# Kernel tuning notes

Hardware: AMD Instinct MI355X
Metric: run time of the kernel (lower is better)

The kernel has to match this reference:

```python
import jax, jax.numpy as jnp
import numpy as np


def setup_inputs() -> dict:
    key = jax.random.key(0)
    ks = jax.random.split(key, 8)
    B, L, E, U = 32, 2048, 1024, 1024
    s = 0.02
    return {
        "dec_hidden": jax.random.normal(ks[0], (B, E), jnp.float32),
        "enc_output": jax.random.normal(ks[1], (B, L, E), jnp.float32),
        "prev_coverage": jax.random.uniform(ks[2], (B, L, 1), jnp.float32),
        "Ws_k": jax.random.normal(ks[3], (E, U), jnp.float32) * s,
        "Ws_b": jnp.zeros((U,), jnp.float32),
        "Wh_k": jax.random.normal(ks[4], (E, U), jnp.float32) * s,
        "Wh_b": jnp.zeros((U,), jnp.float32),
        "Wc_k": jax.random.normal(ks[5], (1, U), jnp.float32) * s,
        "Wc_b": jnp.zeros((U,), jnp.float32),
        "V_k": jax.random.normal(ks[6], (U, 1), jnp.float32) * s,
        "V_b": jnp.zeros((1,), jnp.float32),
        "enc_pad_mask": jnp.ones((B, L), jnp.int32),
        "use_coverage": 1,
    }


def reference(dec_hidden, enc_output, prev_coverage, Ws_k, Ws_b, Wh_k, Wh_b,
              Wc_k, Wc_b, V_k, V_b, enc_pad_mask, use_coverage):
    # projections: [B,L,U] + [B,1,U] (+ [B,L,U] coverage term)
    pre = jnp.einsum('ble,eu->blu', enc_output, Ws_k) + Ws_b \
        + (dec_hidden @ Wh_k + Wh_b)[:, None, :]
    if use_coverage:
        pre = pre + (prev_coverage @ Wc_k + Wc_b)
    score = jnp.tanh(pre) @ V_k + V_b              # [B, L, 1]
    mask = enc_pad_mask.astype(score.dtype)        # [B, L]
    masked_score = (score[..., 0] * mask)[..., None]  # [B, L, 1]
    attention_weights = jax.nn.softmax(masked_score, axis=1)
    coverage = attention_weights + prev_coverage if use_coverage else attention_weights
    context_vector = jnp.sum(attention_weights * enc_output, axis=1)  # [B, E]
    return (context_vector, attention_weights, coverage)
```

## Files before the change

### kernel.cpp

```cpp
#include <hip/hip_runtime.h>
#include <hip/hip_bf16.h>
#include <math.h>

typedef float f32x4 __attribute__((ext_vector_type(4)));
typedef short short8 __attribute__((ext_vector_type(8)));
typedef unsigned short u16x8 __attribute__((ext_vector_type(8)));

static __device__ __forceinline__ unsigned short f2bf(float f) {
    unsigned u = __builtin_bit_cast(unsigned, f);
    unsigned r = (u + 0x7FFFu + ((u >> 16) & 1u)) >> 16;
    return (unsigned short)r;
}
static __device__ __forceinline__ float bf2f(unsigned short h) {
    unsigned u = ((unsigned)h) << 16;
    return __builtin_bit_cast(float, u);
}
static __device__ __forceinline__ float fast_tanh(float x) {
    float ax = fminf(fmaxf(x, -9.f), 9.f);
    float e = __expf(2.f * ax);
    return 1.f - 2.f / (e + 1.f);
}

#define GLD16(g, l) __builtin_amdgcn_global_load_lds(                        \
    (const __attribute__((address_space(1))) void*)(g),                      \
    (__attribute__((address_space(3))) void*)(l), 16, 0, 0)

__global__ __launch_bounds__(256) void prep_kernel(
    const float* __restrict__ enc, unsigned short* __restrict__ encB,
    const float* __restrict__ ws, unsigned short* __restrict__ wst,
    const float* __restrict__ dh, const float* __restrict__ whk,
    float* __restrict__ base_part)
{
    __shared__ unsigned short tile[64][65];
    __shared__ float dS[128];
    const int bid = blockIdx.x, tid = threadIdx.x;

    if (bid < 16384) {
        const size_t base0 = (size_t)bid * 4096;
#pragma unroll
        for (int i = 0; i < 4; i++) {
            size_t g = base0 + (size_t)i * 1024 + tid * 4;
            f32x4 v = *(const f32x4*)(enc + g);
            ushort4 w;
            w.x = f2bf(v.x); w.y = f2bf(v.y); w.z = f2bf(v.z); w.w = f2bf(v.w);
            *(ushort4*)(encB + g) = w;
        }
    } else if (bid < 16640) {
        const int b2 = bid - 16384;
        const int e0 = (b2 & 15) * 64, u0 = (b2 >> 4) * 64;
#pragma unroll
        for (int i = 0; i < 16; i++) {
            int idx = i * 256 + tid;
            int r = idx >> 6, c = idx & 63;
            tile[r][c] = f2bf(ws[(size_t)(e0 + r) * 1024 + u0 + c]);
        }
        __syncthreads();
#pragma unroll
        for (int i = 0; i < 16; i++) {
            int idx = i * 256 + tid;
            int r = idx >> 6, c = idx & 63;
            wst[(size_t)(u0 + r) * 1024 + e0 + c] = tile[c][r];
        }
    } else {
        const int b3 = bid - 16640;
        const int b = b3 & 31, ec = b3 >> 5;
        const int e0 = ec * 128;
        if (tid < 128) dS[tid] = dh[b * 1024 + e0 + tid];
        __syncthreads();
        f32x4 acc = {0.f, 0.f, 0.f, 0.f};
#pragma unroll 4
        for (int e = 0; e < 128; e++)
            acc += dS[e] * *(const f32x4*)(whk + (size_t)(e0 + e) * 1024 + tid * 4);
        *(f32x4*)(base_part + (size_t)ec * 32768 + b * 1024 + tid * 4) = acc;
    }
}

#define SBAR()  __builtin_amdgcn_sched_barrier(0)
#define BARR()  __builtin_amdgcn_s_barrier()
#define PRIO1() __builtin_amdgcn_s_setprio(1)
#define PRIO0() __builtin_amdgcn_s_setprio(0)
#define VMC8()  asm volatile("s_waitcnt vmcnt(8)" ::: "memory")
#define VMC0()  asm volatile("s_waitcnt vmcnt(0)" ::: "memory")

__global__ __launch_bounds__(512, 2) void score_gemm_8ph(
    const unsigned short* __restrict__ encB,
    const unsigned short* __restrict__ wst,
    const float* __restrict__ base_part,
    const float* __restrict__ cov,
    const float* __restrict__ wc,
    const float* __restrict__ vk,
    const float* __restrict__ wsb, const float* __restrict__ whb,
    const float* __restrict__ wcb,
    const int* __restrict__ ucov,
    float* __restrict__ score_part)
{
    __shared__ __align__(16) unsigned short As[2][16384];
    __shared__ __align__(16) unsigned short Bs[2][16384];

    const int tid = threadIdx.x;
    const int bid = blockIdx.x;
    const int sidx = bid >> 3;
    const int row_blk = (bid & 7) * 32 + (sidx >> 2);
    const int u_blk = sidx & 3;
    const int row0 = row_blk << 8;
    const int u0 = u_blk << 8;

    const int lane = tid & 63;
    const int wid  = tid >> 6;
    const int wm = wid >> 2, wn = wid & 3;
    const int l16 = lane & 15, quad = lane >> 4;

    const int k8 = (lane & 7) ^ (lane >> 3);
    unsigned offA[2][2], offB[2][2];
    int dstA[2][2], dstB[2][2];
#pragma unroll
    for (int g = 0; g < 2; g++) {
        const int uu = wid * 2 + g;
#pragma unroll
        for (int h = 0; h < 2; h++) {
            const int ra = ((uu & 8) << 4) + (h << 6) + ((uu & 7) << 3);
            const int rb = ((uu >> 2) << 6) + (h << 5) + ((uu & 3) << 3);
            dstA[g][h] = ra * 64 + lane * 8;
            dstB[g][h] = rb * 64 + lane * 8;
            offA[g][h] = (unsigned)(row0 + ra + (lane >> 3)) * 1024u + (unsigned)(k8 * 8);
            offB[g][h] = (unsigned)(u0 + rb + (lane >> 3)) * 1024u + (unsigned)(k8 * 8);
        }
    }

    const int aBase = (wm * 128 + l16) * 64;
    const int bBase = (wn * 64 + l16) * 64;
    const int ch0 = ((quad) ^ (l16 & 7)) * 8;
    const int ch1 = ((4 + quad) ^ (l16 & 7)) * 8;

#define STAGE_A(bf, h, kt) do {                                             \
    GLD16(encB + offA[0][h] + ((kt) << 6), &As[bf][dstA[0][h]]);            \
    GLD16(encB + offA[1][h] + ((kt) << 6), &As[bf][dstA[1][h]]); } while (0)
#define STAGE_B(bf, h, kt) do {                                             \
    GLD16(wst + offB[0][h] + ((kt) << 6), &Bs[bf][dstB[0][h]]);             \
    GLD16(wst + offB[1][h] + ((kt) << 6), &Bs[bf][dstB[1][h]]); } while (0)

    f32x4 acc[8][4] = {};
    short8 aF[4][2], bF0[2][2], bF1[2][2];

#define LOAD_AF(bf, r) do {                                                 \
    _Pragma("unroll")                                                       \
    for (int fi = 0; fi < 4; fi++) {                                        \
        aF[fi][0] = *(const short8*)&As[bf][aBase + (r)*4096 + fi*1024 + ch0]; \
        aF[fi][1] = *(const short8*)&As[bf][aBase + (r)*4096 + fi*1024 + ch1]; \
    } } while (0)
#define LOAD_BF(bf, c, BF) do {                                             \
    _Pragma("unroll")                                                       \
    for (int fj = 0; fj < 2; fj++) {                                        \
        BF[fj][0] = *(const short8*)&Bs[bf][bBase + (c)*2048 + fj*1024 + ch0]; \
        BF[fj][1] = *(const short8*)&Bs[bf][bBase + (c)*2048 + fj*1024 + ch1]; \
    } } while (0)
#define MFMA16(r, c, BF) do {                                               \
    _Pragma("unroll")                                                       \
    for (int ks = 0; ks < 2; ks++)                                          \
    _Pragma("unroll")                                                       \
    for (int fi = 0; fi < 4; fi++)                                          \
    _Pragma("unroll")                                                       \
    for (int fj = 0; fj < 2; fj++)                                          \
        acc[(r)*4+fi][(c)*2+fj] = __builtin_amdgcn_mfma_f32_16x16x32_bf16(  \
            aF[fi][ks], BF[fj][ks], acc[(r)*4+fi][(c)*2+fj], 0, 0, 0);      \
    } while (0)

    STAGE_A(0, 0, 0);
    STAGE_B(0, 0, 0);
    STAGE_B(0, 1, 0);
    STAGE_A(0, 1, 0);
    STAGE_A(1, 0, 1);
    STAGE_B(1, 0, 1);
    STAGE_B(1, 1, 1);

#pragma unroll 1
    for (int i = 0; i < 7; i++) {
        const int t1 = 2 * i + 1, t2 = 2 * i + 2, t3 = 2 * i + 3;
        STAGE_A(1, 1, t1);
        VMC8();
        SBAR(); BARR(); SBAR();
        LOAD_AF(0, 0); LOAD_BF(0, 0, bF0);
        PRIO1(); MFMA16(0, 0, bF0); PRIO0();
        SBAR(); BARR(); SBAR();
        LOAD_BF(0, 1, bF1);
        STAGE_A(0, 0, t2);
        SBAR(); BARR(); SBAR();
        PRIO1(); MFMA16(0, 1, bF1); PRIO0();
        SBAR(); BARR(); SBAR();
        LOAD_AF(0, 1);
        STAGE_B(0, 0, t2);
        SBAR(); BARR(); SBAR();
        PRIO1(); MFMA16(1, 0, bF0); PRIO0();
        SBAR(); BARR(); SBAR();
        STAGE_B(0, 1, t2);
        SBAR(); BARR(); SBAR();
        PRIO1(); MFMA16(1, 1, bF1); PRIO0();
        SBAR(); BARR(); SBAR();
        STAGE_A(0, 1, t2);
        VMC8();
        SBAR(); BARR(); SBAR();
        LOAD_AF(1, 0); LOAD_BF(1, 0, bF0);
        PRIO1(); MFMA16(0, 0, bF0); PRIO0();
        SBAR(); BARR(); SBAR();
        LOAD_BF(1, 1, bF1);
        STAGE_A(1, 0, t3);
        SBAR(); BARR(); SBAR();
        PRIO1(); MFMA16(0, 1, bF1); PRIO0();
        SBAR(); BARR(); SBAR();
        LOAD_AF(1, 1);
        STAGE_B(1, 0, t3);
        SBAR(); BARR(); SBAR();
        PRIO1(); MFMA16(1, 0, bF0); PRIO0();
        SBAR(); BARR(); SBAR();
        STAGE_B(1, 1, t3);
        SBAR(); BARR(); SBAR();
        PRIO1(); MFMA16(1, 1, bF1); PRIO0();
        SBAR(); BARR(); SBAR();
    }

    STAGE_A(1, 1, 15);
    VMC8();
    SBAR(); BARR(); SBAR();
    LOAD_AF(0, 0); LOAD_BF(0, 0, bF0);
    PRIO1(); MFMA16(0, 0, bF0); PRIO0();
    SBAR(); BARR(); SBAR();
    LOAD_BF(0, 1, bF1);
    SBAR(); BARR(); SBAR();
    PRIO1(); MFMA16(0, 1, bF1); PRIO0();
    SBAR(); BARR(); SBAR();
    LOAD_AF(0, 1);
    SBAR(); BARR(); SBAR();
    PRIO1(); MFMA16(1, 0, bF0); PRIO0();
    PRIO1(); MFMA16(1, 1, bF1); PRIO0();
    VMC0();
    SBAR(); BARR(); SBAR();
    LOAD_AF(1, 0); LOAD_BF(1, 0, bF0);
    PRIO1(); MFMA16(0, 0, bF0); PRIO0();
    LOAD_BF(1, 1, bF1);
    PRIO1(); MFMA16(0, 1, bF1); PRIO0();
    LOAD_AF(1, 1);
    PRIO1(); MFMA16(1, 0, bF0); PRIO0();
    PRIO1(); MFMA16(1, 1, bF1); PRIO0();

    const int use_cov = *ucov;
    const int b = row0 >> 11;
    float baseR[4], wcR[4], vvR[4];
#pragma unroll
    for (int cf = 0; cf < 4; cf++) {
        int u = u0 + wn * 64 + cf * 16 + l16;
        float s = wsb[u] + whb[u] + (use_cov ? wcb[u] : 0.f);
#pragma unroll
        for (int p = 0; p < 8; p++) s += base_part[p * 32768 + b * 1024 + u];
        baseR[cf] = s;
        wcR[cf] = use_cov ? wc[u] : 0.f;
        vvR[cf] = vk[u];
    }
    float* sred = (float*)&Bs[0][0];
#pragma unroll
    for (int rf = 0; rf < 8; rf++) {
        float part[4] = {0.f, 0.f, 0.f, 0.f};
#pragma unroll
        for (int j = 0; j < 4; j++) {
            int rl = wm * 128 + rf * 16 + quad * 4 + j;
            float cvv = use_cov ? cov[row0 + rl] : 0.f;
#pragma unroll
            for (int cf = 0; cf < 4; cf++) {
                float pre = acc[rf][cf][j] + baseR[cf] + cvv * wcR[cf];
                part[j] += fast_tanh(pre) * vvR[cf];
            }
        }
#pragma unroll
        for (int j = 0; j < 4; j++) {
            float v = part[j];
            v += __shfl_xor(v, 1);
            v += __shfl_xor(v, 2);
            v += __shfl_xor(v, 4);
            v += __shfl_xor(v, 8);
            if (l16 == 0) sred[wn * 256 + wm * 128 + rf * 16 + quad * 4 + j] = v;
        }
    }
    __syncthreads();
    if (tid < 256)
        score_part[(size_t)u_blk * 65536 + row0 + tid] =
            sred[tid] + sred[256 + tid] + sred[512 + tid] + sred[768 + tid];

#undef STAGE_A
#undef STAGE_B
#undef LOAD_AF
#undef LOAD_BF
#undef MFMA16
}

__global__ __launch_bounds__(1024) void softmax_kernel(
    const float* __restrict__ score_part, int nplanes,
    const float* __restrict__ vb,
    const int* __restrict__ mask, const float* __restrict__ cov,
    const int* __restrict__ ucov,
    float* __restrict__ attn_out, float* __restrict__ cov_out)
{
    __shared__ float redA[16], redB[16];
    __shared__ float bc0, bc1;
    const int b = blockIdx.x, tid = threadIdx.x;
    const int i0 = b * 2048 + tid, i1 = i0 + 1024;
    const float vbv = vb[0];
    const int uc = *ucov;

    float s0 = 0.f, s1 = 0.f;
    for (int p = 0; p < nplanes; p++) {
        s0 += score_part[(size_t)p * 65536 + i0];
        s1 += score_part[(size_t)p * 65536 + i1];
    }
    s0 = (s0 + vbv) * (float)mask[i0];
    s1 = (s1 + vbv) * (float)mask[i1];

    float m = fmaxf(s0, s1);
#pragma unroll
    for (int off = 1; off < 64; off <<= 1) m = fmaxf(m, __shfl_xor(m, off));
    if ((tid & 63) == 0) redA[tid >> 6] = m;
    __syncthreads();
    if (tid < 16) {
        float v = redA[tid];
#pragma unroll
        for (int off = 1; off < 16; off <<= 1) v = fmaxf(v, __shfl_xor(v, off));
        if (tid == 0) bc0 = v;
    }
    __syncthreads();
    const float M = bc0;

    float e0 = __expf(s0 - M), e1 = __expf(s1 - M);
    float s = e0 + e1;
#pragma unroll
    for (int off = 1; off < 64; off <<= 1) s += __shfl_xor(s, off);
    if ((tid & 63) == 0) redB[tid >> 6] = s;
    __syncthreads();
    if (tid < 16) {
        float v = redB[tid];
#pragma unroll
        for (int off = 1; off < 16; off <<= 1) v += __shfl_xor(v, off);
        if (tid == 0) bc1 = v;
    }
    __syncthreads();
    const float inv = 1.f / bc1;

    float a0 = e0 * inv, a1 = e1 * inv;
    attn_out[i0] = a0;
    attn_out[i1] = a1;
    cov_out[i0] = a0 + (uc ? cov[i0] : 0.f);
    cov_out[i1] = a1 + (uc ? cov[i1] : 0.f);
}

__global__ __launch_bounds__(256) void context_bf16(const unsigned short* __restrict__ encB,
                                                    const float* __restrict__ attn,
                                                    float* __restrict__ out_ctx) {
    __shared__ float aS[2048];
    __shared__ float red[4][64];
    const int b = blockIdx.x, ec = blockIdx.y, tid = threadIdx.x;
    const int e0 = ec * 64;
    for (int i = tid; i < 2048; i += 256) aS[i] = attn[b * 2048 + i];
    __syncthreads();
    const int es = (tid & 7) * 8;
    const int lo = tid >> 3;
    float acc[8] = {};
    for (int l = lo; l < 2048; l += 32) {
        u16x8 w = *(const u16x8*)(encB + (size_t)(b * 2048 + l) * 1024 + e0 + es);
        float a = aS[l];
#pragma unroll
        for (int j = 0; j < 8; j++) acc[j] = fmaf(a, bf2f(w[j]), acc[j]);
    }
#pragma unroll
    for (int j = 0; j < 8; j++) {
        float v = acc[j];
        v += __shfl_xor(v, 8);
        v += __shfl_xor(v, 16);
        v += __shfl_xor(v, 32);
        acc[j] = v;
    }
    const int wv = tid >> 6;
    if ((tid & 63) < 8) {
#pragma unroll
        for (int j = 0; j < 8; j++) red[wv][(tid & 7) * 8 + j] = acc[j];
    }
    __syncthreads();
    if (tid < 64)
        out_ctx[b * 1024 + e0 + tid] = red[0][tid] + red[1][tid] + red[2][tid] + red[3][tid];
}

#define BM 128
#define BN 128
#define BK 32
#define LDT 40
__global__ __launch_bounds__(256) void score_gemm_f32(
    const float* __restrict__ enc, const unsigned short* __restrict__ wst,
    const float* __restrict__ base_part, const float* __restrict__ cov,
    const float* __restrict__ wc, const float* __restrict__ vk,
    const float* __restrict__ wsb, const float* __restrict__ whb,
    const float* __restrict__ wcb,
    const int* __restrict__ ucov, float* __restrict__ score)
{
    __shared__ unsigned short As[BM * LDT];
    __shared__ unsigned short Bs[BN * LDT];
    __shared__ float covS[BM];
    __shared__ float baseS[BN], wcS[BN], vvS[BN];
    const int tid = threadIdx.x;
    const int row0 = blockIdx.x * BM, u0 = blockIdx.y * BN;
    const int b = row0 >> 11;
    const int use_cov = *ucov;
    if (tid < BM) covS[tid] = use_cov ? cov[row0 + tid] : 0.f;
    if (tid < BN) {
        int u = u0 + tid;
        float s = wsb[u] + whb[u] + (use_cov ? wcb[u] : 0.f);
#pragma unroll
        for (int p = 0; p < 8; p++) s += base_part[p * 32768 + b * 1024 + u];
        baseS[tid] = s;
        wcS[tid] = use_cov ? wc[u] : 0.f;
        vvS[tid] = vk[u];
    }
    const int lane = tid & 63, wid = tid >> 6;
    const int wm = wid >> 1, wn = wid & 1;
    const int l16 = lane & 15, quad = lane >> 4;
    f32x4 acc[4][4] = {};
    for (int k0 = 0; k0 < 1024; k0 += BK) {
        __syncthreads();
#pragma unroll
        for (int i = 0; i < 4; i++) {
            int f = i * 256 + tid;
            int r = f >> 3, c4 = f & 7;
            const float* p = enc + (size_t)(row0 + r) * 1024 + k0 + c4 * 4;
            ushort4 w;
            w.x = f2bf(p[0]); w.y = f2bf(p[1]); w.z = f2bf(p[2]); w.w = f2bf(p[3]);
            *(ushort4*)&As[r * LDT + c4 * 4] = w;
        }
#pragma unroll
        for (int i = 0; i < 2; i++) {
            int f = i * 256 + tid;
            int r = f >> 2, c8 = f & 3;
            uint4 w = *(const uint4*)(wst + (size_t)(u0 + r) * 1024 + k0 + c8 * 8);
            *(uint4*)&Bs[r * LDT + c8 * 8] = w;
        }
        __syncthreads();
        short8 a[4], bb[4];
#pragma unroll
        for (int t = 0; t < 4; t++) {
            a[t]  = *(const short8*)&As[(wm * 64 + t * 16 + l16) * LDT + quad * 8];
            bb[t] = *(const short8*)&Bs[(wn * 64 + t * 16 + l16) * LDT + quad * 8];
        }
#pragma unroll
        for (int i = 0; i < 4; i++)
#pragma unroll
            for (int j = 0; j < 4; j++)
                acc[i][j] = __builtin_amdgcn_mfma_f32_16x16x32_bf16(a[i], bb[j], acc[i][j], 0, 0, 0);
    }
#pragma unroll
    for (int i = 0; i < 4; i++) {
        float part[4] = {0.f, 0.f, 0.f, 0.f};
#pragma unroll
        for (int r = 0; r < 4; r++) {
            float cv = covS[wm * 64 + i * 16 + quad * 4 + r];
#pragma unroll
            for (int j = 0; j < 4; j++) {
                int ul = wn * 64 + j * 16 + l16;
                part[r] += fast_tanh(acc[i][j][r] + baseS[ul] + cv * wcS[ul]) * vvS[ul];
            }
        }
#pragma unroll
        for (int r = 0; r < 4; r++) {
            float v = part[r];
            v += __shfl_xor(v, 1);
            v += __shfl_xor(v, 2);
            v += __shfl_xor(v, 4);
            v += __shfl_xor(v, 8);
            if (l16 == 0)
                atomicAdd(&score[row0 + wm * 64 + i * 16 + quad * 4 + r], v);
        }
    }
}

__global__ __launch_bounds__(256) void context_f32(const float* __restrict__ enc,
                                                   const float* __restrict__ attn,
                                                   float* __restrict__ ctx) {
    __shared__ float aS[128];
    const int b = blockIdx.x, lc = blockIdx.y, tid = threadIdx.x;
    const int l0 = lc * 128;
    if (tid < 128) aS[tid] = attn[b * 2048 + l0 + tid];
    __syncthreads();
    const float* p = enc + ((size_t)(b * 2048 + l0)) * 1024 + tid * 4;
    f32x4 acc = {0.f, 0.f, 0.f, 0.f};
#pragma unroll 4
    for (int l = 0; l < 128; l++) acc += *(const f32x4*)(p + (size_t)l * 1024) * aS[l];
    float* o = ctx + b * 1024 + tid * 4;
    atomicAdd(o + 0, acc.x);
    atomicAdd(o + 1, acc.y);
    atomicAdd(o + 2, acc.z);
    atomicAdd(o + 3, acc.w);
}

__global__ __launch_bounds__(256) void prep2_kernel(
    const float* __restrict__ ws, unsigned short* __restrict__ wst,
    const float* __restrict__ dh, const float* __restrict__ whk,
    float* __restrict__ base_part)
{
    __shared__ unsigned short tile[64][65];
    __shared__ float dS[128];
    const int bid = blockIdx.x, tid = threadIdx.x;
    if (bid < 256) {
        const int e0 = (bid & 15) * 64, u0 = (bid >> 4) * 64;
#pragma unroll
        for (int i = 0; i < 16; i++) {
            int idx = i * 256 + tid;
            int r = idx >> 6, c = idx & 63;
            tile[r][c] = f2bf(ws[(size_t)(e0 + r) * 1024 + u0 + c]);
        }
        __syncthreads();
#pragma unroll
        for (int i = 0; i < 16; i++) {
            int idx = i * 256 + tid;
            int r = idx >> 6, c = idx & 63;
            wst[(size_t)(u0 + r) * 1024 + e0 + c] = tile[c][r];
        }
    } else {
        const int b3 = bid - 256;
        const int b = b3 & 31, ec = b3 >> 5;
        const int e0 = ec * 128;
        if (tid < 128) dS[tid] = dh[b * 1024 + e0 + tid];
        __syncthreads();
        f32x4 acc = {0.f, 0.f, 0.f, 0.f};
#pragma unroll 4
        for (int e = 0; e < 128; e++)
            acc += dS[e] * *(const f32x4*)(whk + (size_t)(e0 + e) * 1024 + tid * 4);
        *(f32x4*)(base_part + (size_t)ec * 32768 + b * 1024 + tid * 4) = acc;
    }
}

extern "C" void kernel_launch(void* const* d_in, const int* in_sizes, int n_in,
                              void* d_out, int out_size, void* d_ws, size_t ws_size,
                              hipStream_t stream) {
    const float* dec_hidden = (const float*)d_in[0];
    const float* enc        = (const float*)d_in[1];
    const float* prev_cov   = (const float*)d_in[2];
    const float* Ws_k       = (const float*)d_in[3];
    const float* Ws_b       = (const float*)d_in[4];
    const float* Wh_k       = (const float*)d_in[5];
    const float* Wh_b       = (const float*)d_in[6];
    const float* Wc_k       = (const float*)d_in[7];
    const float* Wc_b       = (const float*)d_in[8];
    const float* V_k        = (const float*)d_in[9];
    const float* V_b        = (const float*)d_in[10];
    const int*   mask       = (const int*)d_in[11];
    const int*   ucov       = (const int*)d_in[12];

    float* out_ctx  = (float*)d_out;
    float* out_attn = out_ctx + 32 * 1024;
    float* out_cov  = out_attn + 65536;

    char* ws = (char*)d_ws;
    unsigned short* wst = (unsigned short*)ws;
    float* base_part  = (float*)(ws + 2097152);
    float* score_part = (float*)(ws + 3145728);
    unsigned short* encB = (unsigned short*)(ws + 5242880);
    const size_t need_fast = 5242880 + (size_t)32 * 2048 * 1024 * 2;

    if (ws_size >= need_fast) {
        prep_kernel<<<16896, 256, 0, stream>>>(enc, encB, Ws_k, wst, dec_hidden, Wh_k, base_part);
        score_gemm_8ph<<<dim3(1024), dim3(512), 0, stream>>>(
            encB, wst, base_part, prev_cov, Wc_k, V_k, Ws_b, Wh_b, Wc_b, ucov, score_part);
        softmax_kernel<<<32, 1024, 0, stream>>>(score_part, 4, V_b, mask, prev_cov, ucov, out_attn, out_cov);
        context_bf16<<<dim3(32, 16), 256, 0, stream>>>(encB, out_attn, out_ctx);
    } else {
        hipMemsetAsync(score_part, 0, 65536 * sizeof(float), stream);
        hipMemsetAsync(out_ctx, 0, 32 * 1024 * sizeof(float), stream);
        prep2_kernel<<<512, 256, 0, stream>>>(Ws_k, wst, dec_hidden, Wh_k, base_part);
        score_gemm_f32<<<dim3(512, 8), 256, 0, stream>>>(
            enc, wst, base_part, prev_cov, Wc_k, V_k, Ws_b, Wh_b, Wc_b, ucov, score_part);
        softmax_kernel<<<32, 1024, 0, stream>>>(score_part, 1, V_b, mask, prev_cov, ucov, out_attn, out_cov);
        context_f32<<<dim3(32, 16), 256, 0, stream>>>(enc, out_attn, out_ctx);
    }
}
```

Measured before the change: 629.7 us.

## Restructure GEMM main loop into four barrier phases with coarser staging

Rewrites the software-pipelined main loop of the score GEMM. It drops from roughly sixteen barrier-separated phases per iteration to four, loads both B fragments up front, and batches MFMA blocks and global-to-LDS stages together. The goal is less barrier and sched_barrier overhead and more freedom for the compiler to interleave memory and MFMA work. The vmcnt waits are re-tuned (6/4) to match the new staging order. This removes the explicit scheduling fences, so the compiler may reorder in ways that hurt overlap, and any mistake in the wait counts risks a race.

```diff
diff --git a/kernel.cpp b/kernel.cpp
--- a/kernel.cpp
+++ b/kernel.cpp
@@ -75,11 +75,11 @@
     }
 }
 
-#define SBAR()  __builtin_amdgcn_sched_barrier(0)
-#define BARR()  __builtin_amdgcn_s_barrier()
+#define BARRM() asm volatile("s_barrier" ::: "memory")
 #define PRIO1() __builtin_amdgcn_s_setprio(1)
 #define PRIO0() __builtin_amdgcn_s_setprio(0)
-#define VMC8()  asm volatile("s_waitcnt vmcnt(8)" ::: "memory")
+#define VMC6()  asm volatile("s_waitcnt vmcnt(6)" ::: "memory")
+#define VMC4()  asm volatile("s_waitcnt vmcnt(4)" ::: "memory")
 #define VMC0()  asm volatile("s_waitcnt vmcnt(0)" ::: "memory")
 
 __global__ __launch_bounds__(512, 2) void score_gemm_8ph(
@@ -172,75 +172,45 @@
     STAGE_A(1, 0, 1);
     STAGE_B(1, 0, 1);
     STAGE_B(1, 1, 1);
+    VMC6();
+    BARRM();
 
 #pragma unroll 1
     for (int i = 0; i < 7; i++) {
         const int t1 = 2 * i + 1, t2 = 2 * i + 2, t3 = 2 * i + 3;
+        LOAD_AF(0, 0); LOAD_BF(0, 0, bF0); LOAD_BF(0, 1, bF1);
         STAGE_A(1, 1, t1);
-        VMC8();
-        SBAR(); BARR(); SBAR();
-        LOAD_AF(0, 0); LOAD_BF(0, 0, bF0);
-        PRIO1(); MFMA16(0, 0, bF0); PRIO0();
-        SBAR(); BARR(); SBAR();
-        LOAD_BF(0, 1, bF1);
-        STAGE_A(0, 0, t2);
-        SBAR(); BARR(); SBAR();
-        PRIO1(); MFMA16(0, 1, bF1); PRIO0();
-        SBAR(); BARR(); SBAR();
+        PRIO1(); MFMA16(0, 0, bF0); MFMA16(0, 1, bF1); PRIO0();
+        BARRM();
         LOAD_AF(0, 1);
-        STAGE_B(0, 0, t2);
-        SBAR(); BARR(); SBAR();
-        PRIO1(); MFMA16(1, 0, bF0); PRIO0();
-        SBAR(); BARR(); SBAR();
-        STAGE_B(0, 1, t2);
-        SBAR(); BARR(); SBAR();
-        PRIO1(); MFMA16(1, 1, bF1); PRIO0();
-        SBAR(); BARR(); SBAR();
-        STAGE_A(0, 1, t2);
-        VMC8();
-        SBAR(); BARR(); SBAR();
-        LOAD_AF(1, 0); LOAD_BF(1, 0, bF0);
-        PRIO1(); MFMA16(0, 0, bF0); PRIO0();
-        SBAR(); BARR(); SBAR();
-        LOAD_BF(1, 1, bF1);
-        STAGE_A(1, 0, t3);
-        SBAR(); BARR(); SBAR();
-        PRIO1(); MFMA16(0, 1, bF1); PRIO0();
-        SBAR(); BARR(); SBAR();
+        STAGE_A(0, 0, t2); STAGE_B(0, 0, t2);
+        PRIO1(); MFMA16(1, 0, bF0); MFMA16(1, 1, bF1); PRIO0();
+        VMC4();
+        BARRM();
+        LOAD_AF(1, 0); LOAD_BF(1, 0, bF0); LOAD_BF(1, 1, bF1);
+        STAGE_B(0, 1, t2); STAGE_A(0, 1, t2);
+        PRIO1(); MFMA16(0, 0, bF0); MFMA16(0, 1, bF1); PRIO0();
+        BARRM();
         LOAD_AF(1, 1);
-        STAGE_B(1, 0, t3);
-        SBAR(); BARR(); SBAR();
-        PRIO1(); MFMA16(1, 0, bF0); PRIO0();
-        SBAR(); BARR(); SBAR();
-        STAGE_B(1, 1, t3);
-        SBAR(); BARR(); SBAR();
-        PRIO1(); MFMA16(1, 1, bF1); PRIO0();
-        SBAR(); BARR(); SBAR();
-    }
-
+        STAGE_A(1, 0, t3); STAGE_B(1, 0, t3); STAGE_B(1, 1, t3);
+        PRIO1(); MFMA16(1, 0, bF0); MFMA16(1, 1, bF1); PRIO0();
+        VMC6();
+        BARRM();
+    }
+
+    LOAD_AF(0, 0); LOAD_BF(0, 0, bF0); LOAD_BF(0, 1, bF1);
     STAGE_A(1, 1, 15);
-    VMC8();
-    SBAR(); BARR(); SBAR();
-    LOAD_AF(0, 0); LOAD_BF(0, 0, bF0);
-    PRIO1(); MFMA16(0, 0, bF0); PRIO0();
-    SBAR(); BARR(); SBAR();
-    LOAD_BF(0, 1, bF1);
-    SBAR(); BARR(); SBAR();
-    PRIO1(); MFMA16(0, 1, bF1); PRIO0();
-    SBAR(); BARR(); SBAR();
+    PRIO1(); MFMA16(0, 0, bF0); MFMA16(0, 1, bF1); PRIO0();
+    BARRM();
     LOAD_AF(0, 1);
-    SBAR(); BARR(); SBAR();
-    PRIO1(); MFMA16(1, 0, bF0); PRIO0();
-    PRIO1(); MFMA16(1, 1, bF1); PRIO0();
+    PRIO1(); MFMA16(1, 0, bF0); MFMA16(1, 1, bF1); PRIO0();
     VMC0();
-    SBAR(); BARR(); SBAR();
-    LOAD_AF(1, 0); LOAD_BF(1, 0, bF0);
-    PRIO1(); MFMA16(0, 0, bF0); PRIO0();
-    LOAD_BF(1, 1, bF1);
-    PRIO1(); MFMA16(0, 1, bF1); PRIO0();
+    BARRM();
+    LOAD_AF(1, 0); LOAD_BF(1, 0, bF0); LOAD_BF(1, 1, bF1);
+    PRIO1(); MFMA16(0, 0, bF0); MFMA16(0, 1, bF1); PRIO0();
+    BARRM();
     LOAD_AF(1, 1);
-    PRIO1(); MFMA16(1, 0, bF0); PRIO0();
-    PRIO1(); MFMA16(1, 1, bF1); PRIO0();
+    PRIO1(); MFMA16(1, 0, bF0); MFMA16(1, 1, bF1); PRIO0();
 
     const int use_cov = *ucov;
     const int b = row0 >> 11;
```

After: 592.5 us. 1.06x faster.
